# Kernel tuning notes

Hardware: AMD Instinct MI355X
Metric: run time of the kernel (lower is better)

The kernel has to match this reference:

```python
import jax, jax.numpy as jnp
import numpy as np

NUM_USERS = 100000
EMB = 128
B = 4096
K = 64


def setup_inputs() -> dict:
    key = jax.random.key(0)
    ks = jax.random.split(key, 8)
    s = 1.0 / np.sqrt(EMB)
    return {
        "node_idx": jax.random.randint(ks[0], (B,), 0, NUM_USERS),
        "neigh_idx": jax.random.randint(ks[1], (B, K), 0, NUM_USERS),
        "neigh_len": jax.random.randint(ks[2], (B,), 0, K + 1),
        "u2e_visual": jax.random.normal(ks[3], (NUM_USERS, EMB), jnp.float32),
        "u2e_text": jax.random.normal(ks[4], (NUM_USERS, EMB), jnp.float32),
        "att_w1": jax.random.normal(ks[5], (2 * EMB, EMB), jnp.float32) * s,
        "att_b1": jnp.zeros((EMB,), jnp.float32),
        "att_w2": jax.random.normal(ks[6], (EMB, EMB), jnp.float32) * s,
        "att_b2": jnp.zeros((EMB,), jnp.float32),
        "att_w3": jax.random.normal(ks[7], (EMB, 1), jnp.float32) * s,
        "att_b3": jnp.zeros((1,), jnp.float32),
    }


def _attend_aggregate(node_rep, neigh_feat, mask, w1, b1, w2, b2, w3, b3):
    # node_rep [B,D], neigh_feat [B,K,D], mask [B,K] bool
    Bn, Kn, D = neigh_feat.shape
    node_b = jnp.broadcast_to(node_rep[:, None, :], (Bn, Kn, D))
    x = jnp.concatenate([neigh_feat, node_b], axis=-1)        # [B,K,2D]
    h = jax.nn.relu(x @ w1 + b1)                              # [B,K,D]
    h = jax.nn.relu(h @ w2 + b2)                              # [B,K,D]
    scores = (h @ w3 + b3)[..., 0]                            # [B,K]
    scores = jnp.where(mask, scores, jnp.float32(-1e30))
    att = jax.nn.softmax(scores, axis=-1)                     # [B,K]
    agg = jnp.einsum('bk,bkd->bd', att, neigh_feat)           # weighted sum
    has_neigh = mask.any(axis=-1, keepdims=True)              # empty list -> self rep
    return jnp.where(has_neigh, agg, node_rep)


def reference(node_idx, neigh_idx, neigh_len, u2e_visual, u2e_text,
              att_w1, att_b1, att_w2, att_b2, att_w3, att_b3):
    mask = jnp.arange(K)[None, :] < neigh_len[:, None]        # [B,K]
    u_v = u2e_visual[node_idx]                                # [B,D]
    u_t = u2e_text[node_idx]                                  # [B,D]
    n_v = u2e_visual[neigh_idx]                               # [B,K,D]
    n_t = u2e_text[neigh_idx]                                 # [B,K,D]
    v_agg = _attend_aggregate(u_v, n_v, mask, att_w1, att_b1, att_w2, att_b2, att_w3, att_b3)
    t_agg = _attend_aggregate(u_t, n_t, mask, att_w1, att_b1, att_w2, att_b2, att_w3, att_b3)
    # (u_v_embed_matrix, u_t_embed_matrix, v_embed_matrix, t_embed_matrix), stacked
    return jnp.stack([u_v, u_t, v_agg, t_agg], axis=0)        # [4,B,D]
```

## Files before the change

kernel.cpp:

```cpp
#include <hip/hip_runtime.h>
#include <math.h>

#define NB 4096
#define KN 64
#define DIM 128
#define HP 132

typedef __bf16 bf16;
typedef bf16 bf16x8 __attribute__((ext_vector_type(8)));
typedef bf16 bf16x4 __attribute__((ext_vector_type(4)));
typedef float f32x4 __attribute__((ext_vector_type(4)));

__global__ void prep_weights(const float* __restrict__ w1,
                             const float* __restrict__ w2,
                             bf16* __restrict__ w1T,
                             bf16* __restrict__ w2T) {
    int t = blockIdx.x * 256 + threadIdx.x;
    if (t < 128 * 256) {
        int j = t >> 8, i = t & 255;
        w1T[t] = (bf16)w1[i * 128 + j];
    } else {
        int t2 = t - 128 * 256;
        int j2 = t2 >> 7, j1 = t2 & 127;
        w2T[t2] = (bf16)w2[j1 * 128 + j2];
    }
}

__global__ __launch_bounds__(256, 4) void graphsage_mfma(
    const int* __restrict__ node_idx,
    const int* __restrict__ neigh_idx,
    const int* __restrict__ neigh_len,
    const float* __restrict__ emb_v,
    const float* __restrict__ emb_t,
    const bf16* __restrict__ w1T,
    const float* __restrict__ b1,
    const bf16* __restrict__ w2T,
    const float* __restrict__ b2,
    const float* __restrict__ w3,
    float* __restrict__ out)
{
    __shared__ bf16  n_lds[KN][HP];
    __shared__ bf16  h1_lds[KN][HP];
    __shared__ float u_lds[DIM];
    __shared__ float part_lds[2][DIM];
    __shared__ float scratch[4][DIM];
    __shared__ float att_lds[KN];
    __shared__ int   ni_lds[KN];

    const int b   = blockIdx.x;
    const int m   = blockIdx.y;
    const int tid = threadIdx.x;
    const int len = neigh_len[b];
    const int nd  = node_idx[b];
    const float* __restrict__ emb = m ? emb_t : emb_v;

    if (tid < DIM) {
        float uv = emb[(size_t)nd * DIM + tid];
        out[((size_t)m * NB + b) * DIM + tid] = uv;
        if (len == 0)
            out[((size_t)(2 + m) * NB + b) * DIM + tid] = uv;
        u_lds[tid] = uv;
    } else if (tid < DIM + KN) {
        ni_lds[tid - DIM] = neigh_idx[b * KN + (tid - DIM)];
    }
    if (len == 0) return;
    __syncthreads();

    const int wv = tid >> 6;
    const int ll = tid & 15;
    const int lh = (tid >> 4) & 3;
    const int nkt = (len + 15) >> 4;
    const int lim = nkt * 16;
    const f32x4 zero4 = {0.f, 0.f, 0.f, 0.f};

    for (int c = tid; c < lim * 16; c += 256) {
        int r = c >> 4, c8 = c & 15;
        bf16x8 v;
        if (r < len) {
            const float* src = emb + (size_t)ni_lds[r] * DIM + c8 * 8;
            float4 f0 = ((const float4*)src)[0];
            float4 f1 = ((const float4*)src)[1];
            v[0] = (bf16)f0.x; v[1] = (bf16)f0.y; v[2] = (bf16)f0.z; v[3] = (bf16)f0.w;
            v[4] = (bf16)f1.x; v[5] = (bf16)f1.y; v[6] = (bf16)f1.z; v[7] = (bf16)f1.w;
        } else {
            #pragma unroll
            for (int q = 0; q < 8; ++q) v[q] = (bf16)0.f;
        }
        *(bf16x8*)&n_lds[r][c8 * 8] = v;
    }
    {
        int j = tid & 127, h = tid >> 7;
        const bf16* wb = w1T + (size_t)j * 256 + DIM + h * 64;
        const float* us = &u_lds[h * 64];
        float a = 0.f;
        #pragma unroll
        for (int i = 0; i < 64; i += 8) {
            bf16x8 w = *(const bf16x8*)(wb + i);
            #pragma unroll
            for (int q = 0; q < 8; ++q) a = fmaf(us[i + q], (float)w[q], a);
        }
        part_lds[h][j] = a;
    }
    __syncthreads();

    {
        bf16x8 af0[4], af1[4];
        #pragma unroll
        for (int ks = 0; ks < 4; ++ks) {
            af0[ks] = *(const bf16x8*)(w1T + (size_t)(wv * 32 + ll) * 256 + ks * 32 + lh * 8);
            af1[ks] = *(const bf16x8*)(w1T + (size_t)(wv * 32 + 16 + ll) * 256 + ks * 32 + lh * 8);
        }
        float4 b1q0 = *(const float4*)(b1 + wv * 32 + lh * 4);
        float4 b1q1 = *(const float4*)(b1 + wv * 32 + 16 + lh * 4);
        float4 p0a = *(const float4*)&part_lds[0][wv * 32 + lh * 4];
        float4 p1a = *(const float4*)&part_lds[1][wv * 32 + lh * 4];
        float4 p0b = *(const float4*)&part_lds[0][wv * 32 + 16 + lh * 4];
        float4 p1b = *(const float4*)&part_lds[1][wv * 32 + 16 + lh * 4];
        float uq0[4] = {p0a.x + p1a.x + b1q0.x, p0a.y + p1a.y + b1q0.y,
                        p0a.z + p1a.z + b1q0.z, p0a.w + p1a.w + b1q0.w};
        float uq1[4] = {p0b.x + p1b.x + b1q1.x, p0b.y + p1b.y + b1q1.y,
                        p0b.z + p1b.z + b1q1.z, p0b.w + p1b.w + b1q1.w};

        #pragma unroll
        for (int kt = 0; kt < 4; ++kt) {
            if (kt < nkt) {
                bf16x8 bfr[4];
                #pragma unroll
                for (int ks = 0; ks < 4; ++ks)
                    bfr[ks] = *(const bf16x8*)&n_lds[kt * 16 + ll][ks * 32 + lh * 8];
                f32x4 a0 = zero4, a1 = zero4;
                #pragma unroll
                for (int ks = 0; ks < 4; ++ks) {
                    a0 = __builtin_amdgcn_mfma_f32_16x16x32_bf16(af0[ks], bfr[ks], a0, 0, 0, 0);
                    a1 = __builtin_amdgcn_mfma_f32_16x16x32_bf16(af1[ks], bfr[ks], a1, 0, 0, 0);
                }
                bf16x4 h0, h1v;
                #pragma unroll
                for (int r = 0; r < 4; ++r) {
                    h0[r]  = (bf16)fmaxf(a0[r] + uq0[r], 0.f);
                    h1v[r] = (bf16)fmaxf(a1[r] + uq1[r], 0.f);
                }
                *(bf16x4*)&h1_lds[kt * 16 + ll][wv * 32 + lh * 4]      = h0;
                *(bf16x4*)&h1_lds[kt * 16 + ll][wv * 32 + 16 + lh * 4] = h1v;
            }
        }
    }
    __syncthreads();

    {
        bf16x8 af20[4], af21[4];
        #pragma unroll
        for (int ks = 0; ks < 4; ++ks) {
            af20[ks] = *(const bf16x8*)(w2T + (size_t)(wv * 32 + ll) * 128 + ks * 32 + lh * 8);
            af21[ks] = *(const bf16x8*)(w2T + (size_t)(wv * 32 + 16 + ll) * 128 + ks * 32 + lh * 8);
        }
        float4 w3a = *(const float4*)(w3 + wv * 32 + lh * 4);
        float4 w3b = *(const float4*)(w3 + wv * 32 + 16 + lh * 4);
        float4 b2a = *(const float4*)(b2 + wv * 32 + lh * 4);
        float4 b2b = *(const float4*)(b2 + wv * 32 + 16 + lh * 4);
        float w3q0[4] = {w3a.x, w3a.y, w3a.z, w3a.w};
        float w3q1[4] = {w3b.x, w3b.y, w3b.z, w3b.w};
        float b2q0[4] = {b2a.x, b2a.y, b2a.z, b2a.w};
        float b2q1[4] = {b2b.x, b2b.y, b2b.z, b2b.w};

        #pragma unroll
        for (int ntk = 0; ntk < 4; ++ntk) {
            if (ntk < nkt) {
                bf16x8 bfr[4];
                #pragma unroll
                for (int ks = 0; ks < 4; ++ks)
                    bfr[ks] = *(const bf16x8*)&h1_lds[ntk * 16 + ll][ks * 32 + lh * 8];
                f32x4 c0 = zero4, c1 = zero4;
                #pragma unroll
                for (int ks = 0; ks < 4; ++ks) {
                    c0 = __builtin_amdgcn_mfma_f32_16x16x32_bf16(af20[ks], bfr[ks], c0, 0, 0, 0);
                    c1 = __builtin_amdgcn_mfma_f32_16x16x32_bf16(af21[ks], bfr[ks], c1, 0, 0, 0);
                }
                float s = 0.f;
                #pragma unroll
                for (int r = 0; r < 4; ++r) {
                    s = fmaf(fmaxf(c0[r] + b2q0[r], 0.f), w3q0[r], s);
                    s = fmaf(fmaxf(c1[r] + b2q1[r], 0.f), w3q1[r], s);
                }
                s += __shfl_xor(s, 16);
                s += __shfl_xor(s, 32);
                if (lh == 0) scratch[wv][ntk * 16 + ll] = s;
            }
        }
    }
    __syncthreads();

    if (tid < KN) {
        float s = scratch[0][tid] + scratch[1][tid] + scratch[2][tid] + scratch[3][tid];
        float sv = (tid < len) ? s : -INFINITY;
        float mx = sv;
        #pragma unroll
        for (int off = 1; off < 64; off <<= 1) mx = fmaxf(mx, __shfl_xor(mx, off));
        float e = (tid < len) ? __expf(sv - mx) : 0.f;
        float sum = e;
        #pragma unroll
        for (int off = 1; off < 64; off <<= 1) sum += __shfl_xor(sum, off);
        att_lds[tid] = e / sum;
    }
    __syncthreads();

    {
        int jg = tid & 31, ks = tid >> 5;
        int j0 = jg * 4;
        float ax = 0.f, ay = 0.f, az = 0.f, aw = 0.f;
        int kb = ks * 8, ke = min(len, kb + 8);
        for (int k = kb; k < ke; ++k) {
            float av = att_lds[k];
            bf16x4 nv = *(const bf16x4*)&n_lds[k][j0];
            ax = fmaf(av, (float)nv[0], ax);
            ay = fmaf(av, (float)nv[1], ay);
            az = fmaf(av, (float)nv[2], az);
            aw = fmaf(av, (float)nv[3], aw);
        }
        ax += __shfl_xor(ax, 32);
        ay += __shfl_xor(ay, 32);
        az += __shfl_xor(az, 32);
        aw += __shfl_xor(aw, 32);
        if ((tid & 63) < 32) {
            float4 v4 = {ax, ay, az, aw};
            *(float4*)&scratch[wv][j0] = v4;
        }
    }
    __syncthreads();
    if (tid < DIM)
        out[((size_t)(2 + m) * NB + b) * DIM + tid] =
            scratch[0][tid] + scratch[1][tid] + scratch[2][tid] + scratch[3][tid];
}

extern "C" void kernel_launch(void* const* d_in, const int* in_sizes, int n_in,
                              void* d_out, int out_size, void* d_ws, size_t ws_size,
                              hipStream_t stream) {
    const int*   node_idx  = (const int*)d_in[0];
    const int*   neigh_idx = (const int*)d_in[1];
    const int*   neigh_len = (const int*)d_in[2];
    const float* emb_v     = (const float*)d_in[3];
    const float* emb_t     = (const float*)d_in[4];
    const float* w1        = (const float*)d_in[5];
    const float* b1        = (const float*)d_in[6];
    const float* w2        = (const float*)d_in[7];
    const float* b2        = (const float*)d_in[8];
    const float* w3        = (const float*)d_in[9];
    float* out = (float*)d_out;

    bf16* w1T = (bf16*)d_ws;
    bf16* w2T = (bf16*)d_ws + 128 * 256;

    hipLaunchKernelGGL(prep_weights, dim3(192), dim3(256), 0, stream, w1, w2, w1T, w2T);
    hipLaunchKernelGGL(graphsage_mfma, dim3(NB, 2), dim3(256), 0, stream,
                       node_idx, neigh_idx, neigh_len, emb_v, emb_t,
                       w1T, b1, w2T, b2, w3, out);
}
```

Before: 119.6 us.

## Partition MLP work by neighbor row tile per wave to remove block barriers

```diff
diff --git a/kernel.cpp b/kernel.cpp
--- a/kernel.cpp
+++ b/kernel.cpp
@@ -43,8 +43,8 @@
     __shared__ bf16  h1_lds[KN][HP];
     __shared__ float u_lds[DIM];
     __shared__ float part_lds[2][DIM];
+    __shared__ float s_lds[KN];
     __shared__ float scratch[4][DIM];
-    __shared__ float att_lds[KN];
     __shared__ int   ni_lds[KN];
 
     const int b   = blockIdx.x;
@@ -66,27 +66,29 @@
     if (len == 0) return;
     __syncthreads();
 
-    const int wv = tid >> 6;
+    const int kt = tid >> 6;
+    const int l  = tid & 63;
     const int ll = tid & 15;
     const int lh = (tid >> 4) & 3;
     const int nkt = (len + 15) >> 4;
-    const int lim = nkt * 16;
-    const f32x4 zero4 = {0.f, 0.f, 0.f, 0.f};
-
-    for (int c = tid; c < lim * 16; c += 256) {
-        int r = c >> 4, c8 = c & 15;
-        bf16x8 v;
-        if (r < len) {
-            const float* src = emb + (size_t)ni_lds[r] * DIM + c8 * 8;
-            float4 f0 = ((const float4*)src)[0];
-            float4 f1 = ((const float4*)src)[1];
-            v[0] = (bf16)f0.x; v[1] = (bf16)f0.y; v[2] = (bf16)f0.z; v[3] = (bf16)f0.w;
-            v[4] = (bf16)f1.x; v[5] = (bf16)f1.y; v[6] = (bf16)f1.z; v[7] = (bf16)f1.w;
-        } else {
-            #pragma unroll
-            for (int q = 0; q < 8; ++q) v[q] = (bf16)0.f;
-        }
-        *(bf16x8*)&n_lds[r][c8 * 8] = v;
+
+    if (kt < nkt) {
+        #pragma unroll
+        for (int it = 0; it < 4; ++it) {
+            int r = kt * 16 + it * 4 + (l >> 4);
+            bf16x8 v;
+            if (r < len) {
+                const float* src = emb + (size_t)ni_lds[r] * DIM + ll * 8;
+                float4 f0 = ((const float4*)src)[0];
+                float4 f1 = ((const float4*)src)[1];
+                v[0] = (bf16)f0.x; v[1] = (bf16)f0.y; v[2] = (bf16)f0.z; v[3] = (bf16)f0.w;
+                v[4] = (bf16)f1.x; v[5] = (bf16)f1.y; v[6] = (bf16)f1.z; v[7] = (bf16)f1.w;
+            } else {
+                #pragma unroll
+                for (int q = 0; q < 8; ++q) v[q] = (bf16)0.f;
+            }
+            *(bf16x8*)&n_lds[r][ll * 8] = v;
+        }
     }
     {
         int j = tid & 127, h = tid >> 7;
@@ -103,133 +105,111 @@
     }
     __syncthreads();
 
+    if (kt < nkt) {
+        f32x4 acc[8];
+        #pragma unroll
+        for (int jt = 0; jt < 8; ++jt) { f32x4 z = {0.f, 0.f, 0.f, 0.f}; acc[jt] = z; }
+        #pragma unroll
+        for (int ks = 0; ks < 4; ++ks) {
+            bf16x8 bfr = *(const bf16x8*)&n_lds[kt * 16 + ll][ks * 32 + lh * 8];
+            #pragma unroll
+            for (int jt = 0; jt < 8; ++jt) {
+                bf16x8 af = *(const bf16x8*)(w1T + (size_t)(jt * 16 + ll) * 256 + ks * 32 + lh * 8);
+                acc[jt] = __builtin_amdgcn_mfma_f32_16x16x32_bf16(af, bfr, acc[jt], 0, 0, 0);
+            }
+        }
+        #pragma unroll
+        for (int jt = 0; jt < 8; ++jt) {
+            float4 p0 = *(const float4*)&part_lds[0][jt * 16 + lh * 4];
+            float4 p1 = *(const float4*)&part_lds[1][jt * 16 + lh * 4];
+            float4 bq = *(const float4*)(b1 + jt * 16 + lh * 4);
+            bf16x4 hv;
+            hv[0] = (bf16)fmaxf(acc[jt][0] + p0.x + p1.x + bq.x, 0.f);
+            hv[1] = (bf16)fmaxf(acc[jt][1] + p0.y + p1.y + bq.y, 0.f);
+            hv[2] = (bf16)fmaxf(acc[jt][2] + p0.z + p1.z + bq.z, 0.f);
+            hv[3] = (bf16)fmaxf(acc[jt][3] + p0.w + p1.w + bq.w, 0.f);
+            *(bf16x4*)&h1_lds[kt * 16 + ll][jt * 16 + lh * 4] = hv;
+        }
+
+        f32x4 c[8];
+        #pragma unroll
+        for (int jt = 0; jt < 8; ++jt) {
+            float4 bq = *(const float4*)(b2 + jt * 16 + lh * 4);
+            f32x4 ci = {bq.x, bq.y, bq.z, bq.w};
+            c[jt] = ci;
+        }
+        #pragma unroll
+        for (int ks = 0; ks < 4; ++ks) {
+            bf16x8 bfr = *(const bf16x8*)&h1_lds[kt * 16 + ll][ks * 32 + lh * 8];
+            #pragma unroll
+            for (int jt = 0; jt < 8; ++jt) {
+                bf16x8 af = *(const bf16x8*)(w2T + (size_t)(jt * 16 + ll) * 128 + ks * 32 + lh * 8);
+                c[jt] = __builtin_amdgcn_mfma_f32_16x16x32_bf16(af, bfr, c[jt], 0, 0, 0);
+            }
+        }
+        float s = 0.f;
+        #pragma unroll
+        for (int jt = 0; jt < 8; ++jt) {
+            float4 w3q = *(const float4*)(w3 + jt * 16 + lh * 4);
+            s = fmaf(fmaxf(c[jt][0], 0.f), w3q.x, s);
+            s = fmaf(fmaxf(c[jt][1], 0.f), w3q.y, s);
+            s = fmaf(fmaxf(c[jt][2], 0.f), w3q.z, s);
+            s = fmaf(fmaxf(c[jt][3], 0.f), w3q.w, s);
+        }
+        s += __shfl_xor(s, 16);
+        s += __shfl_xor(s, 32);
+        if (lh == 0) s_lds[kt * 16 + ll] = s;
+    }
+    __syncthreads();
+
+    float sv = (l < len) ? s_lds[l] : -1e30f;
+    float mx = sv;
+    #pragma unroll
+    for (int off = 1; off < 64; off <<= 1) mx = fmaxf(mx, __shfl_xor(mx, off));
+    float e = (l < len) ? __expf(sv - mx) : 0.f;
+    float sum = e;
+    #pragma unroll
+    for (int off = 1; off < 64; off <<= 1) sum += __shfl_xor(sum, off);
+    float attv = e / sum;
+
     {
-        bf16x8 af0[4], af1[4];
-        #pragma unroll
-        for (int ks = 0; ks < 4; ++ks) {
-            af0[ks] = *(const bf16x8*)(w1T + (size_t)(wv * 32 + ll) * 256 + ks * 32 + lh * 8);
-            af1[ks] = *(const bf16x8*)(w1T + (size_t)(wv * 32 + 16 + ll) * 256 + ks * 32 + lh * 8);
-        }
-        float4 b1q0 = *(const float4*)(b1 + wv * 32 + lh * 4);
-        float4 b1q1 = *(const float4*)(b1 + wv * 32 + 16 + lh * 4);
-        float4 p0a = *(const float4*)&part_lds[0][wv * 32 + lh * 4];
-        float4 p1a = *(const float4*)&part_lds[1][wv * 32 + lh * 4];
-        float4 p0b = *(const float4*)&part_lds[0][wv * 32 + 16 + lh * 4];
-        float4 p1b = *(const float4*)&part_lds[1][wv * 32 + 16 + lh * 4];
-        float uq0[4] = {p0a.x + p1a.x + b1q0.x, p0a.y + p1a.y + b1q0.y,
-                        p0a.z + p1a.z + b1q0.z, p0a.w + p1a.w + b1q0.w};
-        float uq1[4] = {p0b.x + p1b.x + b1q1.x, p0b.y + p1b.y + b1q1.y,
-                        p0b.z + p1b.z + b1q1.z, p0b.w + p1b.w + b1q1.w};
-
-        #pragma unroll
-        for (int kt = 0; kt < 4; ++kt) {
-            if (kt < nkt) {
-                bf16x8 bfr[4];
-                #pragma unroll
-                for (int ks = 0; ks < 4; ++ks)
-                    bfr[ks] = *(const bf16x8*)&n_lds[kt * 16 + ll][ks * 32 + lh * 8];
-                f32x4 a0 = zero4, a1 = zero4;
-                #pragma unroll
-                for (int ks = 0; ks < 4; ++ks) {
-                    a0 = __builtin_amdgcn_mfma_f32_16x16x32_bf16(af0[ks], bfr[ks], a0, 0, 0, 0);
-                    a1 = __builtin_amdgcn_mfma_f32_16x16x32_bf16(af1[ks], bfr[ks], a1, 0, 0, 0);
-                }
-                bf16x4 h0, h1v;
-                #pragma unroll
-                for (int r = 0; r < 4; ++r) {
-                    h0[r]  = (bf16)fmaxf(a0[r] + uq0[r], 0.f);
-                    h1v[r] = (bf16)fmaxf(a1[r] + uq1[r], 0.f);
-                }
-                *(bf16x4*)&h1_lds[kt * 16 + ll][wv * 32 + lh * 4]      = h0;
-                *(bf16x4*)&h1_lds[kt * 16 + ll][wv * 32 + 16 + lh * 4] = h1v;
-            }
-        }
-    }
-    __syncthreads();
-
-    {
-        bf16x8 af20[4], af21[4];
-        #pragma unroll
-        for (int ks = 0; ks < 4; ++ks) {
-            af20[ks] = *(const bf16x8*)(w2T + (size_t)(wv * 32 + ll) * 128 + ks * 32 + lh * 8);
-            af21[ks] = *(const bf16x8*)(w2T + (size_t)(wv * 32 + 16 + ll) * 128 + ks * 32 + lh * 8);
-        }
-        float4 w3a = *(const float4*)(w3 + wv * 32 + lh * 4);
-        float4 w3b = *(const float4*)(w3 + wv * 32 + 16 + lh * 4);
-        float4 b2a = *(const float4*)(b2 + wv * 32 + lh * 4);
-        float4 b2b = *(const float4*)(b2 + wv * 32 + 16 + lh * 4);
-        float w3q0[4] = {w3a.x, w3a.y, w3a.z, w3a.w};
-        float w3q1[4] = {w3b.x, w3b.y, w3b.z, w3b.w};
-        float b2q0[4] = {b2a.x, b2a.y, b2a.z, b2a.w};
-        float b2q1[4] = {b2b.x, b2b.y, b2b.z, b2b.w};
-
-        #pragma unroll
-        for (int ntk = 0; ntk < 4; ++ntk) {
-            if (ntk < nkt) {
-                bf16x8 bfr[4];
-                #pragma unroll
-                for (int ks = 0; ks < 4; ++ks)
-                    bfr[ks] = *(const bf16x8*)&h1_lds[ntk * 16 + ll][ks * 32 + lh * 8];
-                f32x4 c0 = zero4, c1 = zero4;
-                #pragma unroll
-                for (int ks = 0; ks < 4; ++ks) {
-                    c0 = __builtin_amdgcn_mfma_f32_16x16x32_bf16(af20[ks], bfr[ks], c0, 0, 0, 0);
-                    c1 = __builtin_amdgcn_mfma_f32_16x16x32_bf16(af21[ks], bfr[ks], c1, 0, 0, 0);
-                }
-                float s = 0.f;
-                #pragma unroll
-                for (int r = 0; r < 4; ++r) {
-                    s = fmaf(fmaxf(c0[r] + b2q0[r], 0.f), w3q0[r], s);
-                    s = fmaf(fmaxf(c1[r] + b2q1[r], 0.f), w3q1[r], s);
-                }
-                s += __shfl_xor(s, 16);
-                s += __shfl_xor(s, 32);
-                if (lh == 0) scratch[wv][ntk * 16 + ll] = s;
-            }
-        }
-    }
-    __syncthreads();
-
-    if (tid < KN) {
-        float s = scratch[0][tid] + scratch[1][tid] + scratch[2][tid] + scratch[3][tid];
-        float sv = (tid < len) ? s : -INFINITY;
-        float mx = sv;
-        #pragma unroll
-        for (int off = 1; off < 64; off <<= 1) mx = fmaxf(mx, __shfl_xor(mx, off));
-        float e = (tid < len) ? __expf(sv - mx) : 0.f;
-        float sum = e;
-        #pragma unroll
-        for (int off = 1; off < 64; off <<= 1) sum += __shfl_xor(sum, off);
-        att_lds[tid] = e / sum;
-    }
-    __syncthreads();
-
-    {
-        int jg = tid & 31, ks = tid >> 5;
-        int j0 = jg * 4;
+        int slice = l >> 5;
+        int j0 = (l & 31) * 4;
         float ax = 0.f, ay = 0.f, az = 0.f, aw = 0.f;
-        int kb = ks * 8, ke = min(len, kb + 8);
-        for (int k = kb; k < ke; ++k) {
-            float av = att_lds[k];
-            bf16x4 nv = *(const bf16x4*)&n_lds[k][j0];
-            ax = fmaf(av, (float)nv[0], ax);
-            ay = fmaf(av, (float)nv[1], ay);
-            az = fmaf(av, (float)nv[2], az);
-            aw = fmaf(av, (float)nv[3], aw);
+        if (kt < nkt) {
+            #pragma unroll
+            for (int q = 0; q < 8; ++q) {
+                int k = kt * 16 + slice * 8 + q;
+                float ak = __shfl(attv, k);
+                bf16x4 nv = *(const bf16x4*)&n_lds[k][j0];
+                ax = fmaf(ak, (float)nv[0], ax);
+                ay = fmaf(ak, (float)nv[1], ay);
+                az = fmaf(ak, (float)nv[2], az);
+                aw = fmaf(ak, (float)nv[3], aw);
+            }
         }
         ax += __shfl_xor(ax, 32);
         ay += __shfl_xor(ay, 32);
         az += __shfl_xor(az, 32);
         aw += __shfl_xor(aw, 32);
-        if ((tid & 63) < 32) {
+        if (l < 32) {
             float4 v4 = {ax, ay, az, aw};
-            *(float4*)&scratch[wv][j0] = v4;
-        }
-    }
-    __syncthreads();
-    if (tid < DIM)
-        out[((size_t)(2 + m) * NB + b) * DIM + tid] =
-            scratch[0][tid] + scratch[1][tid] + scratch[2][tid] + scratch[3][tid];
+            *(float4*)&scratch[kt][j0] = v4;
+        }
+    }
+    __syncthreads();
+
+    if (tid < 32) {
+        float4 a0 = *(const float4*)&scratch[0][tid * 4];
+        float4 a1 = *(const float4*)&scratch[1][tid * 4];
+        float4 a2 = *(const float4*)&scratch[2][tid * 4];
+        float4 a3 = *(const float4*)&scratch[3][tid * 4];
+        float4 o = {a0.x + a1.x + a2.x + a3.x,
+                    a0.y + a1.y + a2.y + a3.y,
+                    a0.z + a1.z + a2.z + a3.z,
+                    a0.w + a1.w + a2.w + a3.w};
+        *(float4*)(out + ((size_t)(2 + m) * NB + b) * DIM + tid * 4) = o;
+    }
 }
 
 extern "C" void kernel_launch(void* const* d_in, const int* in_sizes, int n_in,
```

Result: slower. 245.9 us (+105.6%).
